# Optimization experiments

Measured on AMD Instinct MI355X. Metric: run time of the kernel, lower is better.

The kernel has to match this reference:

```python
import jax, jax.numpy as jnp
import numpy as np

TOP_K = 2

def _expert(x, w1, w2, w3):
    return (jax.nn.silu(x @ w1.T) * (x @ w3.T)) @ w2.T

def setup_inputs() -> dict:
    key = jax.random.key(0)
    ks = jax.random.split(key, 8)
    B, L, D, F, E, S = 4, 2048, 1024, 512, 16, 1
    p = lambda k, shape: (jax.random.normal(k, shape, jnp.float32) * 0.02)
    return {
        "x": jax.random.normal(ks[0], (B, L, D), jnp.float32),
        "gate_w": p(ks[1], (E, D)),
        "expert_bias": jnp.zeros((E,), jnp.float32),
        "sw1": p(ks[2], (S, F, D)),
        "sw2": p(ks[3], (S, D, F)),
        "sw3": p(ks[4], (S, F, D)),
        "ew1": p(ks[5], (E, F, D)),
        "ew2": p(ks[6], (E, D, F)),
        "ew3": p(ks[7], (E, F, D)),
    }

def reference(x, gate_w, expert_bias, sw1, sw2, sw3, ew1, ew2, ew3):
    B, L, D = x.shape
    E = gate_w.shape[0]
    flat_x = x.reshape(-1, D)  # [T, D], T = B*L

    # Shared experts (always-on)
    shared = sum(_expert(flat_x, sw1[i], sw2[i], sw3[i]) for i in range(sw1.shape[0]))

    # Router (eval mode: no jitter noise, no bias update; expert_bias buffer added)
    logits = flat_x @ gate_w.T + expert_bias          # [T, E]
    probs = jax.nn.softmax(logits, axis=-1)
    topw, topi = jax.lax.top_k(probs, TOP_K)          # [T, k]
    topw = topw / jnp.sum(topw, axis=-1, keepdims=True)

    # Routed experts: combine weight per (token, expert); zero weight => zero contribution,
    # identical math to the masked gather/scatter in the original.
    out = jnp.zeros_like(flat_x)
    for e in range(E):  # fixed small structural loop over experts
        cw = jnp.sum(jnp.where(topi == e, topw, 0.0), axis=-1)  # [T]
        out = out + cw[:, None] * _expert(flat_x, ew1[e], ew2[e], ew3[e])

    y = (shared + out).reshape(B, L, D)
    return y, probs
```

## Files before the change

### kernel.cpp

```cpp
#include <hip/hip_runtime.h>

typedef unsigned short u16;
typedef __bf16 bf16_t;
typedef bf16_t bf16x8 __attribute__((ext_vector_type(8)));
typedef float f32x4 __attribute__((ext_vector_type(4)));

#define T_TOK 8192
#define DIM   1024
#define FF    512
#define NE    16
#define RBASE_SHARED (2 * T_TOK)
#define NROWS (RBASE_SHARED + T_TOK)
#define MAXTILES 256
#define NSEG 512

__device__ __forceinline__ u16 f2bf(float f) {
  union { float f; unsigned u; } v; v.f = f;
  unsigned r = v.u + 0x7FFFu + ((v.u >> 16) & 1u);
  return (u16)(r >> 16);
}
__device__ __forceinline__ float bf2f(u16 h) {
  union { unsigned u; float f; } v; v.u = ((unsigned)h) << 16; return v.f;
}
__device__ __forceinline__ int clampi(int v, int lo, int hi) {
  return v < lo ? lo : (v > hi ? hi : v);
}

#define GLL16(g, l) __builtin_amdgcn_global_load_lds( \
    (const __attribute__((address_space(1))) void*)(g), \
    (__attribute__((address_space(3))) void*)(l), 16, 0, 0)

#define WAIT_VM_BARRIER(n) asm volatile("s_waitcnt vmcnt(" #n ")\n\ts_barrier" ::: "memory")
#define BARRIER_ONLY()     asm volatile("s_barrier" ::: "memory")
#define WAIT_LGKM0()       asm volatile("s_waitcnt lgkmcnt(0)" ::: "memory")

#define X4   2097152
#define SW4  131072
#define EW4  2097152
#define TOT4 (X4 + 3 * SW4 + 3 * EW4)

__global__ __launch_bounds__(256) void cvt_all_kernel(
    const float* __restrict__ x, const float* __restrict__ sw1,
    const float* __restrict__ sw2, const float* __restrict__ sw3,
    const float* __restrict__ ew1, const float* __restrict__ ew2,
    const float* __restrict__ ew3,
    u16* __restrict__ xb, u16* __restrict__ sw1b, u16* __restrict__ sw2b,
    u16* __restrict__ sw3b, u16* __restrict__ ew1b, u16* __restrict__ ew2b,
    u16* __restrict__ ew3b) {
  int i = blockIdx.x * 256 + threadIdx.x;
  const float* s; u16* dst; int j;
  if (i < X4)                       { s = x;   dst = xb;   j = i; }
  else if (i < X4 + SW4)            { s = sw1; dst = sw1b; j = i - X4; }
  else if (i < X4 + 2 * SW4)        { s = sw2; dst = sw2b; j = i - (X4 + SW4); }
  else if (i < X4 + 3 * SW4)        { s = sw3; dst = sw3b; j = i - (X4 + 2 * SW4); }
  else if (i < X4 + 3 * SW4 + EW4)      { s = ew1; dst = ew1b; j = i - (X4 + 3 * SW4); }
  else if (i < X4 + 3 * SW4 + 2 * EW4)  { s = ew2; dst = ew2b; j = i - (X4 + 3 * SW4 + EW4); }
  else if (i < TOT4)                    { s = ew3; dst = ew3b; j = i - (X4 + 3 * SW4 + 2 * EW4); }
  else return;
  float4 v = reinterpret_cast<const float4*>(s)[j];
  ushort4 o;
  o.x = f2bf(v.x); o.y = f2bf(v.y); o.z = f2bf(v.z); o.w = f2bf(v.w);
  reinterpret_cast<ushort4*>(dst)[j] = o;
}

__global__ __launch_bounds__(256) void router_kernel(
    const float* __restrict__ x, const float* __restrict__ gw,
    const float* __restrict__ ebias, float* __restrict__ probs,
    int* __restrict__ topi, float* __restrict__ topw, int* __restrict__ cnt_seg) {
  __shared__ int hist[16];
  int tid = threadIdx.x;
  int lane = tid & 63, w = tid >> 6;
  if (tid < 16) hist[tid] = 0;
  __syncthreads();
  const float4* gv = reinterpret_cast<const float4*>(gw);
  for (int it = 0; it < 2; ++it) {
    int t0 = blockIdx.x * 16 + (w + 4 * it) * 2;
    const float4* x0 = reinterpret_cast<const float4*>(x + (size_t)t0 * DIM);
    const float4* x1 = reinterpret_cast<const float4*>(x + (size_t)(t0 + 1) * DIM);
    float4 xa[4], xc[4];
#pragma unroll
    for (int j = 0; j < 4; ++j) { xa[j] = x0[j * 64 + lane]; xc[j] = x1[j * 64 + lane]; }
    float p0[16], p1[16];
#pragma unroll
    for (int e = 0; e < NE; ++e) {
      float s0 = 0.f, s1 = 0.f;
#pragma unroll
      for (int j = 0; j < 4; ++j) {
        float4 g = gv[e * 256 + j * 64 + lane];
        s0 += xa[j].x * g.x + xa[j].y * g.y + xa[j].z * g.z + xa[j].w * g.w;
        s1 += xc[j].x * g.x + xc[j].y * g.y + xc[j].z * g.z + xc[j].w * g.w;
      }
#pragma unroll
      for (int d = 1; d < 64; d <<= 1) { s0 += __shfl_xor(s0, d); s1 += __shfl_xor(s1, d); }
      float b = ebias[e];
      p0[e] = s0 + b; p1[e] = s1 + b;
    }
    float m0 = p0[0], m1 = p1[0];
#pragma unroll
    for (int e = 1; e < NE; ++e) { m0 = fmaxf(m0, p0[e]); m1 = fmaxf(m1, p1[e]); }
    float sum0 = 0.f, sum1 = 0.f;
#pragma unroll
    for (int e = 0; e < NE; ++e) {
      p0[e] = __expf(p0[e] - m0); sum0 += p0[e];
      p1[e] = __expf(p1[e] - m1); sum1 += p1[e];
    }
    float inv0 = 1.f / sum0, inv1 = 1.f / sum1;
#pragma unroll
    for (int e = 0; e < NE; ++e) { p0[e] *= inv0; p1[e] *= inv1; }
    if (lane == 0) {
#pragma unroll
      for (int j = 0; j < 4; ++j)
        reinterpret_cast<float4*>(probs + (size_t)t0 * NE)[j] =
            make_float4(p0[4 * j], p0[4 * j + 1], p0[4 * j + 2], p0[4 * j + 3]);
      float b1 = -1.f, b2 = -1.f; int i1 = 0, i2 = 0;
#pragma unroll
      for (int e = 0; e < NE; ++e) {
        float pe = p0[e];
        if (pe > b1) { b2 = b1; i2 = i1; b1 = pe; i1 = e; }
        else if (pe > b2) { b2 = pe; i2 = e; }
      }
      float ws = b1 + b2;
      reinterpret_cast<int2*>(topi)[t0] = make_int2(i1, i2);
      reinterpret_cast<float2*>(topw)[t0] = make_float2(b1 / ws, b2 / ws);
      atomicAdd(&hist[i1], 1); atomicAdd(&hist[i2], 1);
    }
    if (lane == 1) {
      int t1 = t0 + 1;
#pragma unroll
      for (int j = 0; j < 4; ++j)
        reinterpret_cast<float4*>(probs + (size_t)t1 * NE)[j] =
            make_float4(p1[4 * j], p1[4 * j + 1], p1[4 * j + 2], p1[4 * j + 3]);
      float b1 = -1.f, b2 = -1.f; int i1 = 0, i2 = 0;
#pragma unroll
      for (int e = 0; e < NE; ++e) {
        float pe = p1[e];
        if (pe > b1) { b2 = b1; i2 = i1; b1 = pe; i1 = e; }
        else if (pe > b2) { b2 = pe; i2 = e; }
      }
      float ws = b1 + b2;
      reinterpret_cast<int2*>(topi)[t1] = make_int2(i1, i2);
      reinterpret_cast<float2*>(topw)[t1] = make_float2(b1 / ws, b2 / ws);
      atomicAdd(&hist[i1], 1); atomicAdd(&hist[i2], 1);
    }
  }
  __syncthreads();
  if (tid < 16) cnt_seg[blockIdx.x * 16 + tid] = hist[tid];
}

__global__ __launch_bounds__(256) void scan_kernel(
    const int* __restrict__ cnt_seg, int* __restrict__ cnt, int* __restrict__ offs,
    int* __restrict__ seg_base, int2* __restrict__ tab) {
  __shared__ int chunk_sum[16][16];
  __shared__ int chunk_base[16][16];
  __shared__ int tot[16], off_s[17];
  int tid = threadIdx.x;
  int e = tid & 15, c = tid >> 4;
  int s0 = 0;
  for (int s = 0; s < 32; ++s) s0 += cnt_seg[(c * 32 + s) * 16 + e];
  chunk_sum[c][e] = s0;
  __syncthreads();
  if (tid < 16) {
    int r = 0;
    for (int c2 = 0; c2 < 16; ++c2) { chunk_base[c2][tid] = r; r += chunk_sum[c2][tid]; }
    tot[tid] = r;
  }
  __syncthreads();
  if (tid == 0) {
    int a = 0;
    for (int i = 0; i < 16; ++i) { off_s[i] = a; offs[i] = a; cnt[i] = tot[i]; a += tot[i]; }
    off_s[16] = RBASE_SHARED; offs[16] = RBASE_SHARED;
    int n = 0;
    for (int g = 0; g <= 16 && n < MAXTILES; ++g) {
      int M = (g == 16) ? T_TOK : tot[g];
      for (int m0 = 0; m0 < M && n < MAXTILES; m0 += 128) { tab[n] = make_int2(g, m0); ++n; }
    }
    for (; n < MAXTILES; ++n) tab[n] = make_int2(-1, 0);
  }
  __syncthreads();
  int r = off_s[e] + chunk_base[c][e];
  for (int s = 0; s < 32; ++s) {
    int seg = c * 32 + s;
    seg_base[seg * 16 + e] = r;
    r += cnt_seg[seg * 16 + e];
  }
}

__global__ __launch_bounds__(64) void scatter_kernel(
    const int* __restrict__ topi, const float* __restrict__ topw,
    const int* __restrict__ seg_base,
    int* __restrict__ idx, float* __restrict__ cwl, int* __restrict__ slotmap) {
  __shared__ int ti[16][2]; __shared__ float tw[16][2]; __shared__ int base[16];
  int b = blockIdx.x;
  int tid = threadIdx.x;
  if (tid < 16) {
    int t = b * 16 + tid;
    int2 pp = reinterpret_cast<const int2*>(topi)[t];
    ti[tid][0] = clampi(pp.x, 0, 15); ti[tid][1] = clampi(pp.y, 0, 15);
    float2 ww = reinterpret_cast<const float2*>(topw)[t];
    tw[tid][0] = ww.x; tw[tid][1] = ww.y;
    base[tid] = seg_base[b * 16 + tid];
  }
  __syncthreads();
  if (tid < 32) {
    int l = tid >> 1, s = tid & 1;
    int t = b * 16 + l;
    int e = ti[l][s];
    int rank = 0;
    for (int t2 = 0; t2 < 16; ++t2) {
      if (ti[t2][0] == e && (t2 < l || (t2 == l && 0 < s))) ++rank;
      if (ti[t2][1] == e && (t2 < l)) ++rank;
    }
    int slot = clampi(base[e] + rank, 0, NROWS - 1);
    idx[slot] = t; cwl[slot] = tw[l][s]; slotmap[t * 3 + s] = slot;
  } else if (tid < 48) {
    int l = tid - 32;
    int t = b * 16 + l;
    int sh = RBASE_SHARED + t;
    idx[sh] = t; cwl[sh] = 1.0f; slotmap[t * 3 + 2] = sh;
  }
}

__global__ __launch_bounds__(256) void gemm_silu_kernel(
    const u16* __restrict__ A, const u16* __restrict__ sw1b, const u16* __restrict__ sw3b,
    const u16* __restrict__ ew1b, const u16* __restrict__ ew3b, u16* __restrict__ G,
    const int2* __restrict__ tab, const int* __restrict__ offs,
    const int* __restrict__ cnt, const int* __restrict__ gidx) {
  const int K = DIM;
  int orig = blockIdx.x;
  int xcd = orig & 7, r = orig >> 3;
  int cc = r & 31, s = r >> 5;
  int tileid = xcd + 8 * ((cc + 9 * s) & 31);
  int ny = s;
  int2 te = tab[tileid];
  int e = te.x;
  if (e < 0) return;
  e = clampi(e, 0, NE);
  int m0 = te.y;
  int M = (e == NE) ? T_TOK : cnt[e];
  M = clampi(M, 1, T_TOK);
  int rowbase = clampi(offs[e], 0, NROWS - 1);
  const u16* B1 = (e == NE) ? sw1b : ew1b + (size_t)e * FF * K;
  const u16* B3 = (e == NE) ? sw3b : ew3b + (size_t)e * FF * K;
  int n0 = ny * 128;

  __shared__ u16 As[2 * 4096], B1s[2 * 4096], B3s[2 * 4096];

  int tid = threadIdx.x;
  int lane = tid & 63, wv = tid >> 6;
  int srow = tid >> 2, sg = tid & 3;
  int sk0 = (sg ^ ((srow >> 1) & 3)) * 8;
  int sk1 = (sg ^ (((srow + 64) >> 1) & 3)) * 8;
  int r0 = min(m0 + srow, M - 1);
  int r1 = min(m0 + srow + 64, M - 1);
  int ga0 = clampi(gidx[clampi(rowbase + r0, 0, NROWS - 1)], 0, T_TOK - 1);
  int ga1 = clampi(gidx[clampi(rowbase + r1, 0, NROWS - 1)], 0, T_TOK - 1);
  const u16* Ap0 = A + (size_t)ga0 * K + sk0;
  const u16* Ap1 = A + (size_t)ga1 * K + sk1;
  const u16* B1p0 = B1 + (size_t)(n0 + srow) * K + sk0;
  const u16* B1p1 = B1 + (size_t)(n0 + srow + 64) * K + sk1;
  const u16* B3p0 = B3 + (size_t)(n0 + srow) * K + sk0;
  const u16* B3p1 = B3 + (size_t)(n0 + srow + 64) * K + sk1;
  int st0 = wv * 512, st1 = 2048 + wv * 512;

  int ln15 = lane & 15, qd = lane >> 4;
  int qsw = (qd ^ ((ln15 >> 1) & 3)) * 8;
  int wm = (wv >> 1) * 64, wn = (wv & 1) * 64;
  int aoff = (wm + ln15) * 32 + qsw;
  int boff = (wn + ln15) * 32 + qsw;

  f32x4 acc1[4][4] = {};
  f32x4 acc3[4][4] = {};

  GLL16(Ap0, As + st0);            GLL16(Ap1, As + st1);
  GLL16(B1p0, B1s + st0);          GLL16(B1p1, B1s + st1);
  GLL16(B3p0, B3s + st0);          GLL16(B3p1, B3s + st1);
  GLL16(Ap0 + 32, As + 4096 + st0);    GLL16(Ap1 + 32, As + 4096 + st1);
  GLL16(B1p0 + 32, B1s + 4096 + st0);  GLL16(B1p1 + 32, B1s + 4096 + st1);
  GLL16(B3p0 + 32, B3s + 4096 + st0);  GLL16(B3p1 + 32, B3s + 4096 + st1);

#pragma unroll
  for (int t = 0; t < 30; ++t) {
    const int cur = (t & 1) * 4096;
    WAIT_VM_BARRIER(6);
    bf16x8 af[4], b1f[4], b3f[4];
#pragma unroll
    for (int i = 0; i < 4; ++i) {
      af[i]  = *reinterpret_cast<const bf16x8*>(&As[cur + aoff + i * 512]);
      b1f[i] = *reinterpret_cast<const bf16x8*>(&B1s[cur + boff + i * 512]);
      b3f[i] = *reinterpret_cast<const bf16x8*>(&B3s[cur + boff + i * 512]);
    }
    WAIT_LGKM0();
    __builtin_amdgcn_sched_barrier(0);
    BARRIER_ONLY();
    const int kt = (t + 2) * 32;
    GLL16(Ap0 + kt, As + cur + st0);     GLL16(Ap1 + kt, As + cur + st1);
    GLL16(B1p0 + kt, B1s + cur + st0);   GLL16(B1p1 + kt, B1s + cur + st1);
    GLL16(B3p0 + kt, B3s + cur + st0);   GLL16(B3p1 + kt, B3s + cur + st1);
    __builtin_amdgcn_s_setprio(1);
#pragma unroll
    for (int i = 0; i < 4; ++i)
#pragma unroll
      for (int j = 0; j < 4; ++j) {
        acc1[i][j] = __builtin_amdgcn_mfma_f32_16x16x32_bf16(af[i], b1f[j], acc1[i][j], 0, 0, 0);
        acc3[i][j] = __builtin_amdgcn_mfma_f32_16x16x32_bf16(af[i], b3f[j], acc3[i][j], 0, 0, 0);
      }
    __builtin_amdgcn_s_setprio(0);
  }
  {
    const int cur = 0;
    WAIT_VM_BARRIER(6);
    bf16x8 af[4], b1f[4], b3f[4];
#pragma unroll
    for (int i = 0; i < 4; ++i) {
      af[i]  = *reinterpret_cast<const bf16x8*>(&As[cur + aoff + i * 512]);
      b1f[i] = *reinterpret_cast<const bf16x8*>(&B1s[cur + boff + i * 512]);
      b3f[i] = *reinterpret_cast<const bf16x8*>(&B3s[cur + boff + i * 512]);
    }
    WAIT_LGKM0();
    __builtin_amdgcn_sched_barrier(0);
    __builtin_amdgcn_s_setprio(1);
#pragma unroll
    for (int i = 0; i < 4; ++i)
#pragma unroll
      for (int j = 0; j < 4; ++j) {
        acc1[i][j] = __builtin_amdgcn_mfma_f32_16x16x32_bf16(af[i], b1f[j], acc1[i][j], 0, 0, 0);
        acc3[i][j] = __builtin_amdgcn_mfma_f32_16x16x32_bf16(af[i], b3f[j], acc3[i][j], 0, 0, 0);
      }
    __builtin_amdgcn_s_setprio(0);
  }
  {
    const int cur = 4096;
    WAIT_VM_BARRIER(0);
    bf16x8 af[4], b1f[4], b3f[4];
#pragma unroll
    for (int i = 0; i < 4; ++i) {
      af[i]  = *reinterpret_cast<const bf16x8*>(&As[cur + aoff + i * 512]);
      b1f[i] = *reinterpret_cast<const bf16x8*>(&B1s[cur + boff + i * 512]);
      b3f[i] = *reinterpret_cast<const bf16x8*>(&B3s[cur + boff + i * 512]);
    }
    WAIT_LGKM0();
    __builtin_amdgcn_sched_barrier(0);
    __builtin_amdgcn_s_setprio(1);
#pragma unroll
    for (int i = 0; i < 4; ++i)
#pragma unroll
      for (int j = 0; j < 4; ++j) {
        acc1[i][j] = __builtin_amdgcn_mfma_f32_16x16x32_bf16(af[i], b1f[j], acc1[i][j], 0, 0, 0);
        acc3[i][j] = __builtin_amdgcn_mfma_f32_16x16x32_bf16(af[i], b3f[j], acc3[i][j], 0, 0, 0);
      }
    __builtin_amdgcn_s_setprio(0);
  }

  int mrem = M - m0;
#pragma unroll
  for (int i = 0; i < 4; ++i)
#pragma unroll
    for (int r2 = 0; r2 < 4; ++r2) {
      int ml = wm + i * 16 + qd * 4 + r2;
      if (ml < mrem) {
        size_t orow = (size_t)clampi(rowbase + m0 + ml, 0, NROWS - 1);
#pragma unroll
        for (int j = 0; j < 4; ++j) {
          float z1 = acc1[i][j][r2], z3 = acc3[i][j][r2];
          float g = z1 / (1.f + __expf(-z1)) * z3;
          G[orow * FF + n0 + wn + j * 16 + ln15] = f2bf(g);
        }
      }
    }
}

__global__ __launch_bounds__(256) void gemm_out_kernel(
    const u16* __restrict__ Gb, const u16* __restrict__ sw2b, const u16* __restrict__ ew2b,
    u16* __restrict__ O, const int2* __restrict__ tab, const int* __restrict__ offs,
    const int* __restrict__ cnt, const float* __restrict__ cwl) {
  const int K = FF;
  int orig = blockIdx.x;
  int xcd = orig & 7, r = orig >> 3;
  int cc = r & 31, s = r >> 5;
  int tileid = xcd + 8 * ((cc + 9 * s) & 31);
  int ny = s;
  int2 te = tab[tileid];
  int e = te.x;
  if (e < 0) return;
  e = clampi(e, 0, NE);
  int m0 = te.y;
  int M = (e == NE) ? T_TOK : cnt[e];
  M = clampi(M, 1, T_TOK);
  int rowbase = clampi(offs[e], 0, NROWS - 1);
  const u16* B = (e == NE) ? sw2b : ew2b + (size_t)e * DIM * K;
  int n0 = ny * 128;

  __shared__ u16 As[3 * 4096], Bs[3 * 4096];

  int tid = threadIdx.x;
  int lane = tid & 63, wv = tid >> 6;
  int srow = tid >> 2, sg = tid & 3;
  int sk0 = (sg ^ ((srow >> 1) & 3)) * 8;
  int sk1 = (sg ^ (((srow + 64) >> 1) & 3)) * 8;
  int r0 = clampi(rowbase + min(m0 + srow, M - 1), 0, NROWS - 1);
  int r1 = clampi(rowbase + min(m0 + srow + 64, M - 1), 0, NROWS - 1);
  const u16* Ap0 = Gb + (size_t)r0 * K + sk0;
  const u16* Ap1 = Gb + (size_t)r1 * K + sk1;
  const u16* Bp0 = B + (size_t)(n0 + srow) * K + sk0;
  const u16* Bp1 = B + (size_t)(n0 + srow + 64) * K + sk1;
  int st0 = wv * 512, st1 = 2048 + wv * 512;

  int ln15 = lane & 15, qd = lane >> 4;
  int qsw = (qd ^ ((ln15 >> 1) & 3)) * 8;
  int wm = (wv >> 1) * 64, wn = (wv & 1) * 64;
  int aoff = (wm + ln15) * 32 + qsw;
  int boff = (wn + ln15) * 32 + qsw;

  f32x4 acc[4][4] = {};

  GLL16(Ap0, As + st0);    GLL16(Ap1, As + st1);
  GLL16(Bp0, Bs + st0);    GLL16(Bp1, Bs + st1);
  GLL16(Ap0 + 32, As + 4096 + st0);  GLL16(Ap1 + 32, As + 4096 + st1);
  GLL16(Bp0 + 32, Bs + 4096 + st0);  GLL16(Bp1 + 32, Bs + 4096 + st1);

#pragma unroll
  for (int t = 0; t < 14; ++t) {
    const int cur = (t % 3) * 4096;
    const int nxt = ((t + 2) % 3) * 4096;
    WAIT_VM_BARRIER(4);
    const int kt = (t + 2) * 32;
    GLL16(Ap0 + kt, As + nxt + st0);   GLL16(Ap1 + kt, As + nxt + st1);
    GLL16(Bp0 + kt, Bs + nxt + st0);   GLL16(Bp1 + kt, Bs + nxt + st1);
    bf16x8 af[4], bf[4];
#pragma unroll
    for (int i = 0; i < 4; ++i) {
      af[i] = *reinterpret_cast<const bf16x8*>(&As[cur + aoff + i * 512]);
      bf[i] = *reinterpret_cast<const bf16x8*>(&Bs[cur + boff + i * 512]);
    }
    WAIT_LGKM0();
    __builtin_amdgcn_sched_barrier(0);
    __builtin_amdgcn_s_setprio(1);
#pragma unroll
    for (int i = 0; i < 4; ++i)
#pragma unroll
      for (int j = 0; j < 4; ++j)
        acc[i][j] = __builtin_amdgcn_mfma_f32_16x16x32_bf16(af[i], bf[j], acc[i][j], 0, 0, 0);
    __builtin_amdgcn_s_setprio(0);
  }
  {
    const int cur = (14 % 3) * 4096;
    WAIT_VM_BARRIER(4);
    bf16x8 af[4], bf[4];
#pragma unroll
    for (int i = 0; i < 4; ++i) {
      af[i] = *reinterpret_cast<const bf16x8*>(&As[cur + aoff + i * 512]);
      bf[i] = *reinterpret_cast<const bf16x8*>(&Bs[cur + boff + i * 512]);
    }
    WAIT_LGKM0();
    __builtin_amdgcn_sched_barrier(0);
    __builtin_amdgcn_s_setprio(1);
#pragma unroll
    for (int i = 0; i < 4; ++i)
#pragma unroll
      for (int j = 0; j < 4; ++j)
        acc[i][j] = __builtin_amdgcn_mfma_f32_16x16x32_bf16(af[i], bf[j], acc[i][j], 0, 0, 0);
    __builtin_amdgcn_s_setprio(0);
  }
  {
    const int cur = (15 % 3) * 4096;
    WAIT_VM_BARRIER(0);
    bf16x8 af[4], bf[4];
#pragma unroll
    for (int i = 0; i < 4; ++i) {
      af[i] = *reinterpret_cast<const bf16x8*>(&As[cur + aoff + i * 512]);
      bf[i] = *reinterpret_cast<const bf16x8*>(&Bs[cur + boff + i * 512]);
    }
    WAIT_LGKM0();
    __builtin_amdgcn_sched_barrier(0);
    __builtin_amdgcn_s_setprio(1);
#pragma unroll
    for (int i = 0; i < 4; ++i)
#pragma unroll
      for (int j = 0; j < 4; ++j)
        acc[i][j] = __builtin_amdgcn_mfma_f32_16x16x32_bf16(af[i], bf[j], acc[i][j], 0, 0, 0);
    __builtin_amdgcn_s_setprio(0);
  }

  int mrem = M - m0;
#pragma unroll
  for (int i = 0; i < 4; ++i)
#pragma unroll
    for (int r2 = 0; r2 < 4; ++r2) {
      int ml = wm + i * 16 + qd * 4 + r2;
      if (ml < mrem) {
        int slot = clampi(rowbase + m0 + ml, 0, NROWS - 1);
        float cw = cwl[slot];
#pragma unroll
        for (int j = 0; j < 4; ++j)
          O[(size_t)slot * DIM + n0 + wn + j * 16 + ln15] = f2bf(acc[i][j][r2] * cw);
      }
    }
}

__global__ __launch_bounds__(256) void combine_kernel(
    const u16* __restrict__ O, const int* __restrict__ slotmap, float* __restrict__ y) {
  int t = blockIdx.x;
  int c = threadIdx.x;
  int s0 = clampi(slotmap[t * 3], 0, NROWS - 1);
  int s1 = clampi(slotmap[t * 3 + 1], 0, NROWS - 1);
  int s2 = clampi(slotmap[t * 3 + 2], 0, NROWS - 1);
  ushort4 a = reinterpret_cast<const ushort4*>(O + (size_t)s0 * DIM)[c];
  ushort4 b = reinterpret_cast<const ushort4*>(O + (size_t)s1 * DIM)[c];
  ushort4 d = reinterpret_cast<const ushort4*>(O + (size_t)s2 * DIM)[c];
  float4 r;
  r.x = bf2f(a.x) + bf2f(b.x) + bf2f(d.x);
  r.y = bf2f(a.y) + bf2f(b.y) + bf2f(d.y);
  r.z = bf2f(a.z) + bf2f(b.z) + bf2f(d.z);
  r.w = bf2f(a.w) + bf2f(b.w) + bf2f(d.w);
  reinterpret_cast<float4*>(y + (size_t)t * DIM)[c] = r;
}

extern "C" void kernel_launch(void* const* d_in, const int* in_sizes, int n_in,
                              void* d_out, int out_size, void* d_ws, size_t ws_size,
                              hipStream_t stream) {
  const float* x     = (const float*)d_in[0];
  const float* gw    = (const float*)d_in[1];
  const float* ebias = (const float*)d_in[2];
  const float* sw1   = (const float*)d_in[3];
  const float* sw2   = (const float*)d_in[4];
  const float* sw3   = (const float*)d_in[5];
  const float* ew1   = (const float*)d_in[6];
  const float* ew2   = (const float*)d_in[7];
  const float* ew3   = (const float*)d_in[8];
  float* y = (float*)d_out;
  float* probs = y + (size_t)T_TOK * DIM;

  char* ws = (char*)d_ws;
  size_t o = 0;
  auto alloc = [&](size_t bytes) -> char* {
    char* p = ws + o;
    o = (o + bytes + 255) & ~(size_t)255;
    return p;
  };
  u16* G    = (u16*)alloc((size_t)NROWS * FF * 2);
  u16* sw1b = (u16*)alloc((size_t)FF * DIM * 2);
  u16* sw2b = (u16*)alloc((size_t)FF * DIM * 2);
  u16* sw3b = (u16*)alloc((size_t)FF * DIM * 2);
  u16* ew2b = (u16*)alloc((size_t)NE * FF * DIM * 2);
  char* aliasBase = alloc((size_t)NROWS * DIM * 2);
  u16* xb   = (u16*)aliasBase;
  u16* ew1b = (u16*)(aliasBase + (size_t)T_TOK * DIM * 2);
  u16* ew3b = (u16*)(aliasBase + (size_t)T_TOK * DIM * 2 + (size_t)NE * FF * DIM * 2);
  u16* O    = (u16*)aliasBase;
  int*   topi    = (int*)alloc(T_TOK * 2 * 4);
  float* topw    = (float*)alloc(T_TOK * 2 * 4);
  int*   idx     = (int*)alloc(NROWS * 4);
  float* cwl     = (float*)alloc(NROWS * 4);
  int*   slotmap = (int*)alloc(T_TOK * 3 * 4);
  int2*  tab     = (int2*)alloc(MAXTILES * 8);
  int*   cnt_seg = (int*)alloc(NSEG * 16 * 4);
  int*   seg_base= (int*)alloc(NSEG * 16 * 4);
  int*   cnt     = (int*)alloc(256);
  int*   offs    = (int*)alloc(256);

  router_kernel<<<NSEG, 256, 0, stream>>>(x, gw, ebias, probs, topi, topw, cnt_seg);
  scan_kernel<<<1, 256, 0, stream>>>(cnt_seg, cnt, offs, seg_base, tab);
  scatter_kernel<<<NSEG, 64, 0, stream>>>(topi, topw, seg_base, idx, cwl, slotmap);
  cvt_all_kernel<<<TOT4 / 256, 256, 0, stream>>>(x, sw1, sw2, sw3, ew1, ew2, ew3,
                                                 xb, sw1b, sw2b, sw3b, ew1b, ew2b, ew3b);

  gemm_silu_kernel<<<1024, 256, 0, stream>>>(
      xb, sw1b, sw3b, ew1b, ew3b, G, tab, offs, cnt, idx);
  gemm_out_kernel<<<2048, 256, 0, stream>>>(
      G, sw2b, ew2b, O, tab, offs, cnt, cwl);
  combine_kernel<<<T_TOK, 256, 0, stream>>>(O, slotmap, y);
}
```

Measured before the change: 416.0 us.

## Deepen GEMM LDS pipelines to three stages and split B1/B3 fragment loads

```diff
diff --git a/kernel.cpp b/kernel.cpp
--- a/kernel.cpp
+++ b/kernel.cpp
@@ -220,7 +220,7 @@
   }
 }
 
-__global__ __launch_bounds__(256) void gemm_silu_kernel(
+__global__ __launch_bounds__(256, 2) void gemm_silu_kernel(
     const u16* __restrict__ A, const u16* __restrict__ sw1b, const u16* __restrict__ sw3b,
     const u16* __restrict__ ew1b, const u16* __restrict__ ew3b, u16* __restrict__ G,
     const int2* __restrict__ tab, const int* __restrict__ offs,
@@ -243,7 +243,7 @@
   const u16* B3 = (e == NE) ? sw3b : ew3b + (size_t)e * FF * K;
   int n0 = ny * 128;
 
-  __shared__ u16 As[2 * 4096], B1s[2 * 4096], B3s[2 * 4096];
+  __shared__ u16 As[3 * 4096], B1s[3 * 4096], B3s[3 * 4096];
 
   int tid = threadIdx.x;
   int lane = tid & 63, wv = tid >> 6;
@@ -271,28 +271,41 @@
   f32x4 acc1[4][4] = {};
   f32x4 acc3[4][4] = {};
 
-  GLL16(Ap0, As + st0);            GLL16(Ap1, As + st1);
-  GLL16(B1p0, B1s + st0);          GLL16(B1p1, B1s + st1);
-  GLL16(B3p0, B3s + st0);          GLL16(B3p1, B3s + st1);
-  GLL16(Ap0 + 32, As + 4096 + st0);    GLL16(Ap1 + 32, As + 4096 + st1);
-  GLL16(B1p0 + 32, B1s + 4096 + st0);  GLL16(B1p1 + 32, B1s + 4096 + st1);
-  GLL16(B3p0 + 32, B3s + 4096 + st0);  GLL16(B3p1 + 32, B3s + 4096 + st1);
-
-#pragma unroll
-  for (int t = 0; t < 30; ++t) {
-    const int cur = (t & 1) * 4096;
-    WAIT_VM_BARRIER(6);
-    bf16x8 af[4], b1f[4], b3f[4];
+#pragma unroll
+  for (int b = 0; b < 3; ++b) {
+    const int bb = b * 4096, kb = b * 32;
+    GLL16(Ap0 + kb, As + bb + st0);      GLL16(Ap1 + kb, As + bb + st1);
+    GLL16(B1p0 + kb, B1s + bb + st0);    GLL16(B1p1 + kb, B1s + bb + st1);
+    GLL16(B3p0 + kb, B3s + bb + st0);    GLL16(B3p1 + kb, B3s + bb + st1);
+  }
+
+#pragma unroll
+  for (int t = 0; t < 29; ++t) {
+    const int cur = (t % 3) * 4096;
+    WAIT_VM_BARRIER(12);
+    bf16x8 af[4], bx[4];
 #pragma unroll
     for (int i = 0; i < 4; ++i) {
-      af[i]  = *reinterpret_cast<const bf16x8*>(&As[cur + aoff + i * 512]);
-      b1f[i] = *reinterpret_cast<const bf16x8*>(&B1s[cur + boff + i * 512]);
-      b3f[i] = *reinterpret_cast<const bf16x8*>(&B3s[cur + boff + i * 512]);
+      af[i] = *reinterpret_cast<const bf16x8*>(&As[cur + aoff + i * 512]);
+      bx[i] = *reinterpret_cast<const bf16x8*>(&B1s[cur + boff + i * 512]);
     }
     WAIT_LGKM0();
     __builtin_amdgcn_sched_barrier(0);
+    __builtin_amdgcn_s_setprio(1);
+#pragma unroll
+    for (int i = 0; i < 4; ++i)
+#pragma unroll
+      for (int j = 0; j < 4; ++j)
+        acc1[i][j] = __builtin_amdgcn_mfma_f32_16x16x32_bf16(af[i], bx[j], acc1[i][j], 0, 0, 0);
+    __builtin_amdgcn_s_setprio(0);
+    __builtin_amdgcn_sched_barrier(0);
+#pragma unroll
+    for (int i = 0; i < 4; ++i)
+      bx[i] = *reinterpret_cast<const bf16x8*>(&B3s[cur + boff + i * 512]);
+    WAIT_LGKM0();
+    __builtin_amdgcn_sched_barrier(0);
     BARRIER_ONLY();
-    const int kt = (t + 2) * 32;
+    const int kt = (t + 3) * 32;
     GLL16(Ap0 + kt, As + cur + st0);     GLL16(Ap1 + kt, As + cur + st1);
     GLL16(B1p0 + kt, B1s + cur + st0);   GLL16(B1p1 + kt, B1s + cur + st1);
     GLL16(B3p0 + kt, B3s + cur + st0);   GLL16(B3p1 + kt, B3s + cur + st1);
@@ -300,21 +313,21 @@
 #pragma unroll
     for (int i = 0; i < 4; ++i)
 #pragma unroll
-      for (int j = 0; j < 4; ++j) {
-        acc1[i][j] = __builtin_amdgcn_mfma_f32_16x16x32_bf16(af[i], b1f[j], acc1[i][j], 0, 0, 0);
-        acc3[i][j] = __builtin_amdgcn_mfma_f32_16x16x32_bf16(af[i], b3f[j], acc3[i][j], 0, 0, 0);
-      }
+      for (int j = 0; j < 4; ++j)
+        acc3[i][j] = __builtin_amdgcn_mfma_f32_16x16x32_bf16(af[i], bx[j], acc3[i][j], 0, 0, 0);
     __builtin_amdgcn_s_setprio(0);
   }
-  {
-    const int cur = 0;
-    WAIT_VM_BARRIER(6);
-    bf16x8 af[4], b1f[4], b3f[4];
+#pragma unroll
+  for (int pt = 29; pt < 32; ++pt) {
+    const int cur = (pt % 3) * 4096;
+    if (pt == 29)      { WAIT_VM_BARRIER(12); }
+    else if (pt == 30) { WAIT_VM_BARRIER(6); }
+    else               { WAIT_VM_BARRIER(0); }
+    bf16x8 af[4], bx[4];
 #pragma unroll
     for (int i = 0; i < 4; ++i) {
-      af[i]  = *reinterpret_cast<const bf16x8*>(&As[cur + aoff + i * 512]);
-      b1f[i] = *reinterpret_cast<const bf16x8*>(&B1s[cur + boff + i * 512]);
-      b3f[i] = *reinterpret_cast<const bf16x8*>(&B3s[cur + boff + i * 512]);
+      af[i] = *reinterpret_cast<const bf16x8*>(&As[cur + aoff + i * 512]);
+      bx[i] = *reinterpret_cast<const bf16x8*>(&B1s[cur + boff + i * 512]);
     }
     WAIT_LGKM0();
     __builtin_amdgcn_sched_barrier(0);
@@ -322,32 +335,21 @@
 #pragma unroll
     for (int i = 0; i < 4; ++i)
 #pragma unroll
-      for (int j = 0; j < 4; ++j) {
-        acc1[i][j] = __builtin_amdgcn_mfma_f32_16x16x32_bf16(af[i], b1f[j], acc1[i][j], 0, 0, 0);
-        acc3[i][j] = __builtin_amdgcn_mfma_f32_16x16x32_bf16(af[i], b3f[j], acc3[i][j], 0, 0, 0);
-      }
+      for (int j = 0; j < 4; ++j)
+        acc1[i][j] = __builtin_amdgcn_mfma_f32_16x16x32_bf16(af[i], bx[j], acc1[i][j], 0, 0, 0);
     __builtin_amdgcn_s_setprio(0);
-  }
-  {
-    const int cur = 4096;
-    WAIT_VM_BARRIER(0);
-    bf16x8 af[4], b1f[4], b3f[4];
-#pragma unroll
-    for (int i = 0; i < 4; ++i) {
-      af[i]  = *reinterpret_cast<const bf16x8*>(&As[cur + aoff + i * 512]);
-      b1f[i] = *reinterpret_cast<const bf16x8*>(&B1s[cur + boff + i * 512]);
-      b3f[i] = *reinterpret_cast<const bf16x8*>(&B3s[cur + boff + i * 512]);
-    }
+    __builtin_amdgcn_sched_barrier(0);
+#pragma unroll
+    for (int i = 0; i < 4; ++i)
+      bx[i] = *reinterpret_cast<const bf16x8*>(&B3s[cur + boff + i * 512]);
     WAIT_LGKM0();
     __builtin_amdgcn_sched_barrier(0);
     __builtin_amdgcn_s_setprio(1);
 #pragma unroll
     for (int i = 0; i < 4; ++i)
 #pragma unroll
-      for (int j = 0; j < 4; ++j) {
-        acc1[i][j] = __builtin_amdgcn_mfma_f32_16x16x32_bf16(af[i], b1f[j], acc1[i][j], 0, 0, 0);
-        acc3[i][j] = __builtin_amdgcn_mfma_f32_16x16x32_bf16(af[i], b3f[j], acc3[i][j], 0, 0, 0);
-      }
+      for (int j = 0; j < 4; ++j)
+        acc3[i][j] = __builtin_amdgcn_mfma_f32_16x16x32_bf16(af[i], bx[j], acc3[i][j], 0, 0, 0);
     __builtin_amdgcn_s_setprio(0);
   }
 
@@ -369,7 +371,7 @@
     }
 }
 
-__global__ __launch_bounds__(256) void gemm_out_kernel(
+__global__ __launch_bounds__(256, 2) void gemm_out_kernel(
     const u16* __restrict__ Gb, const u16* __restrict__ sw2b, const u16* __restrict__ ew2b,
     u16* __restrict__ O, const int2* __restrict__ tab, const int* __restrict__ offs,
     const int* __restrict__ cnt, const float* __restrict__ cwl) {
@@ -413,19 +415,17 @@
 
   f32x4 acc[4][4] = {};
 
-  GLL16(Ap0, As + st0);    GLL16(Ap1, As + st1);
-  GLL16(Bp0, Bs + st0);    GLL16(Bp1, Bs + st1);
-  GLL16(Ap0 + 32, As + 4096 + st0);  GLL16(Ap1 + 32, As + 4096 + st1);
-  GLL16(Bp0 + 32, Bs + 4096 + st0);  GLL16(Bp1 + 32, Bs + 4096 + st1);
-
-#pragma unroll
-  for (int t = 0; t < 14; ++t) {
+#pragma unroll
+  for (int b = 0; b < 3; ++b) {
+    const int bb = b * 4096, kb = b * 32;
+    GLL16(Ap0 + kb, As + bb + st0);   GLL16(Ap1 + kb, As + bb + st1);
+    GLL16(Bp0 + kb, Bs + bb + st0);   GLL16(Bp1 + kb, Bs + bb + st1);
+  }
+
+#pragma unroll
+  for (int t = 0; t < 13; ++t) {
     const int cur = (t % 3) * 4096;
-    const int nxt = ((t + 2) % 3) * 4096;
-    WAIT_VM_BARRIER(4);
-    const int kt = (t + 2) * 32;
-    GLL16(Ap0 + kt, As + nxt + st0);   GLL16(Ap1 + kt, As + nxt + st1);
-    GLL16(Bp0 + kt, Bs + nxt + st0);   GLL16(Bp1 + kt, Bs + nxt + st1);
+    WAIT_VM_BARRIER(8);
     bf16x8 af[4], bf[4];
 #pragma unroll
     for (int i = 0; i < 4; ++i) {
@@ -434,6 +434,10 @@
     }
     WAIT_LGKM0();
     __builtin_amdgcn_sched_barrier(0);
+    BARRIER_ONLY();
+    const int kt = (t + 3) * 32;
+    GLL16(Ap0 + kt, As + cur + st0);   GLL16(Ap1 + kt, As + cur + st1);
+    GLL16(Bp0 + kt, Bs + cur + st0);   GLL16(Bp1 + kt, Bs + cur + st1);
     __builtin_amdgcn_s_setprio(1);
 #pragma unroll
     for (int i = 0; i < 4; ++i)
@@ -442,28 +446,12 @@
         acc[i][j] = __builtin_amdgcn_mfma_f32_16x16x32_bf16(af[i], bf[j], acc[i][j], 0, 0, 0);
     __builtin_amdgcn_s_setprio(0);
   }
-  {
-    const int cur = (14 % 3) * 4096;
-    WAIT_VM_BARRIER(4);
-    bf16x8 af[4], bf[4];
-#pragma unroll
-    for (int i = 0; i < 4; ++i) {
-      af[i] = *reinterpret_cast<const bf16x8*>(&As[cur + aoff + i * 512]);
-      bf[i] = *reinterpret_cast<const bf16x8*>(&Bs[cur + boff + i * 512]);
-    }
-    WAIT_LGKM0();
-    __builtin_amdgcn_sched_barrier(0);
-    __builtin_amdgcn_s_setprio(1);
-#pragma unroll
-    for (int i = 0; i < 4; ++i)
-#pragma unroll
-      for (int j = 0; j < 4; ++j)
-        acc[i][j] = __builtin_amdgcn_mfma_f32_16x16x32_bf16(af[i], bf[j], acc[i][j], 0, 0, 0);
-    __builtin_amdgcn_s_setprio(0);
-  }
-  {
-    const int cur = (15 % 3) * 4096;
-    WAIT_VM_BARRIER(0);
+#pragma unroll
+  for (int pt = 13; pt < 16; ++pt) {
+    const int cur = (pt % 3) * 4096;
+    if (pt == 13)      { WAIT_VM_BARRIER(8); }
+    else if (pt == 14) { WAIT_VM_BARRIER(4); }
+    else               { WAIT_VM_BARRIER(0); }
     bf16x8 af[4], bf[4];
 #pragma unroll
     for (int i = 0; i < 4; ++i) {
```

New measurement: 386.6 us. 7.1% less time.
